# Optimization experiments

Measured on AMD Instinct MI355X. Metric: run time of the kernel, lower is better.

Reference implementation:

```python
import jax, jax.numpy as jnp
import numpy as np

N, C, HI, WI = 8, 3, 512, 512   # src_img NCHW (input_img_size)
HO, WO = 2048, 2048             # output canvas (output_img_size[2:])
EPS = 1e-8


def _transform_one(img, coor_row):
    """Replicates: sigmoid box params -> theta -> F.affine_grid -> F.grid_sample
    (bilinear, zeros padding, align_corners=False). Theta has zero off-diagonals,
    so the grid is separable in x/y and the bilinear sample factorizes.
    img: [C, HI, WI]; coor_row: [4]. Returns (sample [C,HO,WO], mask [HO,WO])."""
    x = jax.nn.sigmoid(coor_row[0]) * WO
    y = jax.nn.sigmoid(coor_row[1]) * HO
    w = jax.nn.sigmoid(coor_row[2]) * WO
    h = jax.nn.sigmoid(coor_row[3]) * HO
    a = WO / (w + EPS)
    tx = 2.0 / WO * (WO / 2.0 - x) * a
    b = HO / (h + EPS)
    ty = 2.0 / HO * (HO / 2.0 - y) * b
    # affine_grid base coords (align_corners=False): center-of-pixel normalized
    xs = (2.0 * jnp.arange(WO, dtype=img.dtype) + 1.0) / WO - 1.0
    ys = (2.0 * jnp.arange(HO, dtype=img.dtype) + 1.0) / HO - 1.0
    gx = a * xs + tx          # [WO]
    gy = b * ys + ty          # [HO]
    # grid_sample unnormalize (align_corners=False)
    ix = ((gx + 1.0) * WI - 1.0) / 2.0
    iy = ((gy + 1.0) * HI - 1.0) / 2.0
    x0f = jnp.floor(ix); y0f = jnp.floor(iy)
    wx1 = ix - x0f; wx0 = 1.0 - wx1
    wy1 = iy - y0f; wy0 = 1.0 - wy1
    x0 = x0f.astype(jnp.int32); x1 = x0 + 1
    y0 = y0f.astype(jnp.int32); y1 = y0 + 1
    vx0 = ((x0 >= 0) & (x0 < WI)).astype(img.dtype)
    vx1 = ((x1 >= 0) & (x1 < WI)).astype(img.dtype)
    vy0 = ((y0 >= 0) & (y0 < HI)).astype(img.dtype)
    vy1 = ((y1 >= 0) & (y1 < HI)).astype(img.dtype)
    x0c = jnp.clip(x0, 0, WI - 1); x1c = jnp.clip(x1, 0, WI - 1)
    y0c = jnp.clip(y0, 0, HI - 1); y1c = jnp.clip(y1, 0, HI - 1)
    wyv0 = wy0 * vy0; wyv1 = wy1 * vy1
    wxv0 = wx0 * vx0; wxv1 = wx1 * vx1
    # separable bilinear gather with zero padding
    rows = img[:, y0c, :] * wyv0[None, :, None] + img[:, y1c, :] * wyv1[None, :, None]  # [C,HO,WI]
    samp = rows[:, :, x0c] * wxv0[None, None, :] + rows[:, :, x1c] * wxv1[None, None, :]  # [C,HO,WO]
    # grid_sample of an all-ones mask == sum of in-bounds bilinear weights (separable)
    mask = (wyv0 + wyv1)[:, None] * (wxv0 + wxv1)[None, :]  # [HO,WO]
    return samp, mask


def _composite(src_img, bg_img, coor):
    def step(bg, inp):
        img, c = inp
        s, m = _transform_one(img, c)
        bg = bg * (1.0 - m)[None, None] + (s * m[None])[None]
        return bg, None
    bg, _ = jax.lax.scan(step, bg_img, (src_img, coor))
    return bg


def setup_inputs() -> dict:
    key = jax.random.key(0)
    k1, k2, k3 = jax.random.split(key, 3)
    src_img = jax.random.normal(k1, (N, C, HI, WI), dtype=jnp.float32)
    bg_img = jax.random.uniform(k2, (1, C, HO, WO), dtype=jnp.float32)
    coor = jax.random.normal(k3, (N, 4), dtype=jnp.float32)  # nn.Parameter
    return {"src_img": src_img, "bg_img": bg_img, "coor": coor}


def reference(src_img, bg_img, coor):
    return _composite(src_img, bg_img, coor)
```

## Files before the change

### kernel.cpp

```cpp
#include <hip/hip_runtime.h>

#define WI 512
#define HI 512
#define WO 2048
#define HO 2048
#define NIMG 8
#define CCH 3
#define EPS 1e-8f
#define PLANE (HI * WI)

#define TPB  256
#define SEG  1024
#define PXT  4
#define CAP  520

struct SState {
    float wy0, wy1, my;
    int   t0a, R, lim;
    int   valid;
    int   fc;
};

__device__ __forceinline__ SState calc_state(const float4 P, const float ys,
                                             const int wo0) {
    SState st; st.valid = 0; st.fc = 0; st.wy0 = st.wy1 = st.my = 0.0f;
    st.t0a = 0; st.R = 0; st.lim = 0;
    const float gy  = P.z * ys + P.w;
    const float iy  = ((gy + 1.0f) * (float)HI - 1.0f) * 0.5f;
    const float y0f = floorf(iy);
    const float fy1 = iy - y0f;
    const float fy0 = 1.0f - fy1;
    const float y1f = y0f + 1.0f;
    const float v0  = (y0f >= 0.0f && y0f < (float)HI) ? 1.0f : 0.0f;
    const float v1  = (y1f >= 0.0f && y1f < (float)HI) ? 1.0f : 0.0f;
    st.wy0 = fy0 * v0;
    st.wy1 = fy1 * v1;
    st.my  = st.wy0 + st.wy1;
    if (!(st.my > 0.0f)) return st;

    const float a  = P.x, tx = P.y;
    const float xsf = (2.0f * (float)wo0 + 1.0f) / (float)WO - 1.0f;
    const float xsl = (2.0f * (float)(wo0 + SEG - 1) + 1.0f) / (float)WO - 1.0f;
    const float ixf = ((a * xsf + tx + 1.0f) * (float)WI - 1.0f) * 0.5f;
    const float ixl = ((a * xsl + tx + 1.0f) * (float)WI - 1.0f) * 0.5f;
    if (ixl <= -1.0f || ixf >= (float)WI) return st;

    const int t0 = (int)fminf(fmaxf(floorf(ixf), 0.0f), (float)(WI - 1));
    const int t1 = (int)fminf(fmaxf(floorf(ixl) + 1.0f, 0.0f), (float)(WI - 1));
    st.t0a = t0 & ~3;
    int R = (t1 - st.t0a + 4) & ~3;
    if (R > WI - st.t0a) R = WI - st.t0a;
    st.R   = R;
    st.lim = t1 - st.t0a;
    st.valid = 1;
    st.fc = (st.my == 1.0f) && (ixf >= 0.0f) && (ixl < (float)(WI - 1));
    return st;
}

__launch_bounds__(TPB)
__global__ void diffcomp_v10(const float* __restrict__ src,
                             const float* __restrict__ bg,
                             const float* __restrict__ coor,
                             float* __restrict__ out) {
    __shared__ float  cs[2][CCH][CAP];
    __shared__ float4 prm[NIMG];

    const int tid = threadIdx.x;
    const int b   = blockIdx.x;
    const int row = b >> 1;
    const int wo0 = (b & 1) << 10;

    if (tid < NIMG) {
        const float cx  = coor[tid * 4 + 0];
        const float cy  = coor[tid * 4 + 1];
        const float cw  = coor[tid * 4 + 2];
        const float chh = coor[tid * 4 + 3];
        const float x = (1.0f / (1.0f + expf(-cx))) * (float)WO;
        const float y = (1.0f / (1.0f + expf(-cy))) * (float)HO;
        const float w = (1.0f / (1.0f + expf(-cw))) * (float)WO;
        const float h = (1.0f / (1.0f + expf(-chh))) * (float)HO;
        const float a  = (float)WO / (w + EPS);
        const float tx = (2.0f / (float)WO) * ((float)WO * 0.5f - x) * a;
        const float bb = (float)HO / (h + EPS);
        const float ty = (2.0f / (float)HO) * ((float)HO * 0.5f - y) * bb;
        prm[tid] = make_float4(a, tx, bb, ty);
    }
    __syncthreads();

    const float ys = (2.0f * (float)row + 1.0f) / (float)HO - 1.0f;

    unsigned cov = 0u, fcb = 0u;
#pragma unroll
    for (int n = 0; n < NIMG; n++) {
        const SState s = calc_state(prm[n], ys, wo0);
        if (s.valid) cov |= (1u << n);
        if (s.fc)    fcb |= (1u << n);
    }
    if (fcb) {
        const int j0 = 31 - __builtin_clz(fcb);
        cov &= ~((1u << j0) - 1u);
    }

    float xsv[PXT];
#pragma unroll
    for (int p = 0; p < PXT; p++) {
        const int wo = wo0 + p * TPB + tid;
        xsv[p] = (2.0f * (float)wo + 1.0f) / (float)WO - 1.0f;
    }

    const int base = row * WO + wo0 + tid;
    float acc[CCH][PXT];
    if (fcb == 0u) {
#pragma unroll
        for (int c = 0; c < CCH; c++)
#pragma unroll
            for (int p = 0; p < PXT; p++)
                acc[c][p] = bg[c * HO * WO + base + p * TPB];
    } else {
#pragma unroll
        for (int c = 0; c < CCH; c++)
#pragma unroll
            for (int p = 0; p < PXT; p++)
                acc[c][p] = 0.0f;
    }

    if (cov) {
        float4 A0[CCH], A1[CCH], B0[CCH], B1[CCH];
        SState stA, stB;

        auto load_img = [&](int n, SState& st, float4* r0, float4* r1) {
            st = calc_state(prm[n], ys, wo0);
            const int xo = tid << 2;
            if (xo < st.R) {
                const float* ib = src + n * (CCH * PLANE) + st.t0a + xo;
                const float gy  = prm[n].z * ys + prm[n].w;
                const float iy  = ((gy + 1.0f) * (float)HI - 1.0f) * 0.5f;
                const float y0f = floorf(iy);
                const int y0o = (int)fminf(fmaxf(y0f, 0.0f), (float)(HI - 1)) * WI;
                const int y1o = (int)fminf(fmaxf(y0f + 1.0f, 0.0f), (float)(HI - 1)) * WI;
#pragma unroll
                for (int c = 0; c < CCH; c++) {
                    r0[c] = *(const float4*)(ib + c * PLANE + y0o);
                    r1[c] = *(const float4*)(ib + c * PLANE + y1o);
                }
            }
        };

        auto commit_img = [&](int slot, const SState& st,
                              const float4* r0, const float4* r1) {
            const int xo = tid << 2;
            if (xo < st.R) {
#pragma unroll
                for (int c = 0; c < CCH; c++) {
                    float4 rc;
                    rc.x = r0[c].x * st.wy0 + r1[c].x * st.wy1;
                    rc.y = r0[c].y * st.wy0 + r1[c].y * st.wy1;
                    rc.z = r0[c].z * st.wy0 + r1[c].z * st.wy1;
                    rc.w = r0[c].w * st.wy0 + r1[c].w * st.wy1;
                    *(float4*)&cs[slot][c][xo] = rc;
                }
            }
        };

        auto blend_img = [&](int slot, int n, const SState& st) {
            const float a  = prm[n].x;
            const float tx = prm[n].y;
#pragma unroll
            for (int p = 0; p < PXT; p++) {
                const float gx  = a * xsv[p] + tx;
                const float ix  = ((gx + 1.0f) * (float)WI - 1.0f) * 0.5f;
                const float x0f = floorf(ix);
                const float fx1 = ix - x0f;
                const float fx0 = 1.0f - fx1;
                const float x1f = x0f + 1.0f;
                const float v0  = (x0f >= 0.0f && x0f < (float)WI) ? 1.0f : 0.0f;
                const float v1  = (x1f >= 0.0f && x1f < (float)WI) ? 1.0f : 0.0f;
                const float wx0 = fx0 * v0;
                const float wx1 = fx1 * v1;
                int x0r = (int)fminf(fmaxf(x0f, 0.0f), (float)(WI - 1)) - st.t0a;
                int x1r = (int)fminf(fmaxf(x1f, 0.0f), (float)(WI - 1)) - st.t0a;
                x0r = min(max(x0r, 0), st.lim);
                x1r = min(max(x1r, 0), st.lim);
                const float m  = st.my * (wx0 + wx1);
                const float om = 1.0f - m;
#pragma unroll
                for (int c = 0; c < CCH; c++) {
                    const float q0 = cs[slot][c][x0r];
                    const float q1 = cs[slot][c][x1r];
                    const float sc = q0 * wx0 + q1 * wx1;
                    acc[c][p] = acc[c][p] * om + sc * m;
                }
            }
        };

        int cur = (int)__builtin_ctz(cov);
        unsigned rest = cov & (cov - 1u);

        load_img(cur, stA, A0, A1);
        int s = 0;
        while (true) {
            const int nxt = rest ? (int)__builtin_ctz(rest) : -1;
            if (nxt >= 0) load_img(nxt, stB, B0, B1);
            commit_img(s, stA, A0, A1);
            __syncthreads();
            blend_img(s, cur, stA);
            if (nxt < 0) break;
            cur = nxt;
            rest &= rest - 1u;
            stA = stB;
#pragma unroll
            for (int c = 0; c < CCH; c++) { A0[c] = B0[c]; A1[c] = B1[c]; }
            s ^= 1;
        }
    }

#pragma unroll
    for (int c = 0; c < CCH; c++)
#pragma unroll
        for (int p = 0; p < PXT; p++)
            out[c * HO * WO + base + p * TPB] = acc[c][p];
}

extern "C" void kernel_launch(void* const* d_in, const int* in_sizes, int n_in,
                              void* d_out, int out_size, void* d_ws, size_t ws_size,
                              hipStream_t stream) {
    const float* src  = (const float*)d_in[0];
    const float* bg   = (const float*)d_in[1];
    const float* coor = (const float*)d_in[2];
    float* out = (float*)d_out;
    (void)d_ws; (void)ws_size;

    hipLaunchKernelGGL(diffcomp_v10, dim3(HO * (WO / SEG)), dim3(TPB), 0, stream,
                       src, bg, coor, out);
}
```

Measured before the change: 134.9 us.

## Precompute per-image row state in LDS, vectorize pixel IO, interleave channels

```diff
diff --git a/kernel.cpp b/kernel.cpp
--- a/kernel.cpp
+++ b/kernel.cpp
@@ -14,108 +14,95 @@
 #define PXT  4
 #define CAP  520
 
-struct SState {
-    float wy0, wy1, my;
-    int   t0a, R, lim;
-    int   valid;
-    int   fc;
-};
-
-__device__ __forceinline__ SState calc_state(const float4 P, const float ys,
-                                             const int wo0) {
-    SState st; st.valid = 0; st.fc = 0; st.wy0 = st.wy1 = st.my = 0.0f;
-    st.t0a = 0; st.R = 0; st.lim = 0;
-    const float gy  = P.z * ys + P.w;
-    const float iy  = ((gy + 1.0f) * (float)HI - 1.0f) * 0.5f;
-    const float y0f = floorf(iy);
-    const float fy1 = iy - y0f;
-    const float fy0 = 1.0f - fy1;
-    const float y1f = y0f + 1.0f;
-    const float v0  = (y0f >= 0.0f && y0f < (float)HI) ? 1.0f : 0.0f;
-    const float v1  = (y1f >= 0.0f && y1f < (float)HI) ? 1.0f : 0.0f;
-    st.wy0 = fy0 * v0;
-    st.wy1 = fy1 * v1;
-    st.my  = st.wy0 + st.wy1;
-    if (!(st.my > 0.0f)) return st;
-
-    const float a  = P.x, tx = P.y;
-    const float xsf = (2.0f * (float)wo0 + 1.0f) / (float)WO - 1.0f;
-    const float xsl = (2.0f * (float)(wo0 + SEG - 1) + 1.0f) / (float)WO - 1.0f;
-    const float ixf = ((a * xsf + tx + 1.0f) * (float)WI - 1.0f) * 0.5f;
-    const float ixl = ((a * xsl + tx + 1.0f) * (float)WI - 1.0f) * 0.5f;
-    if (ixl <= -1.0f || ixf >= (float)WI) return st;
-
-    const int t0 = (int)fminf(fmaxf(floorf(ixf), 0.0f), (float)(WI - 1));
-    const int t1 = (int)fminf(fmaxf(floorf(ixl) + 1.0f, 0.0f), (float)(WI - 1));
-    st.t0a = t0 & ~3;
-    int R = (t1 - st.t0a + 4) & ~3;
-    if (R > WI - st.t0a) R = WI - st.t0a;
-    st.R   = R;
-    st.lim = t1 - st.t0a;
-    st.valid = 1;
-    st.fc = (st.my == 1.0f) && (ixf >= 0.0f) && (ixl < (float)(WI - 1));
-    return st;
-}
-
 __launch_bounds__(TPB)
-__global__ void diffcomp_v10(const float* __restrict__ src,
+__global__ void diffcomp_v11(const float* __restrict__ src,
                              const float* __restrict__ bg,
                              const float* __restrict__ coor,
                              float* __restrict__ out) {
-    __shared__ float  cs[2][CCH][CAP];
-    __shared__ float4 prm[NIMG];
+    __shared__ __align__(16) float cs[2][CAP * CCH];
+    __shared__ float4 st1[NIMG];
+    __shared__ float4 st2[NIMG];
+    __shared__ float4 st3[NIMG];
 
     const int tid = threadIdx.x;
-    const int b   = blockIdx.x;
+    const int b0  = blockIdx.x;
+    const int b   = ((b0 & 7) << 9) | (b0 >> 3);
     const int row = b >> 1;
     const int wo0 = (b & 1) << 10;
+    const float ys = (2.0f * (float)row + 1.0f) / (float)HO - 1.0f;
+    const float HW1 = 0.5f * (float)(WI - 1);
 
     if (tid < NIMG) {
         const float cx  = coor[tid * 4 + 0];
         const float cy  = coor[tid * 4 + 1];
         const float cw  = coor[tid * 4 + 2];
         const float chh = coor[tid * 4 + 3];
-        const float x = (1.0f / (1.0f + expf(-cx))) * (float)WO;
-        const float y = (1.0f / (1.0f + expf(-cy))) * (float)HO;
-        const float w = (1.0f / (1.0f + expf(-cw))) * (float)WO;
-        const float h = (1.0f / (1.0f + expf(-chh))) * (float)HO;
+        const float xx = (1.0f / (1.0f + expf(-cx))) * (float)WO;
+        const float yy = (1.0f / (1.0f + expf(-cy))) * (float)HO;
+        const float w  = (1.0f / (1.0f + expf(-cw))) * (float)WO;
+        const float h  = (1.0f / (1.0f + expf(-chh))) * (float)HO;
         const float a  = (float)WO / (w + EPS);
-        const float tx = (2.0f / (float)WO) * ((float)WO * 0.5f - x) * a;
         const float bb = (float)HO / (h + EPS);
-        const float ty = (2.0f / (float)HO) * ((float)HO * 0.5f - y) * bb;
-        prm[tid] = make_float4(a, tx, bb, ty);
+        const float ty = (2.0f / (float)HO) * ((float)HO * 0.5f - yy) * bb;
+
+        const float gy  = bb * ys + ty;
+        const float iy  = ((gy + 1.0f) * (float)HI - 1.0f) * 0.5f;
+        const float y0f = floorf(iy);
+        const float fy1 = iy - y0f;
+        const float fy0 = 1.0f - fy1;
+        const float y1f = y0f + 1.0f;
+        const float v0  = (y0f >= 0.0f && y0f < (float)HI) ? 1.0f : 0.0f;
+        const float v1  = (y1f >= 0.0f && y1f < (float)HI) ? 1.0f : 0.0f;
+        const float wy0 = fy0 * v0;
+        const float wy1 = fy1 * v1;
+        const float my  = wy0 + wy1;
+        const float y0of = fminf(fmaxf(y0f, 0.0f), (float)(HI - 1)) * (float)WI;
+        const float y1of = fminf(fmaxf(y1f, 0.0f), (float)(HI - 1)) * (float)WI;
+
+        const float A2 = a * ((float)WI / (float)WO);
+        const float D  = 0.5f - xx;
+
+        float myv = 0.0f, t0af = 0.0f, limf = 0.0f, Rf = 0.0f, fcf = 0.0f;
+        if (my > 0.0f) {
+            const float ixf = fmaf(A2, (float)wo0 + D, HW1);
+            const float ixl = fmaf(A2, (float)(wo0 + SEG - 1) + D, HW1);
+            if (!(ixl <= -1.0f || ixf >= (float)WI)) {
+                const int t0 = (int)fminf(fmaxf(floorf(ixf), 0.0f), (float)(WI - 1));
+                const int t1 = (int)fminf(fmaxf(floorf(ixl) + 1.0f, 0.0f), (float)(WI - 1));
+                const int t0a = t0 & ~3;
+                int R = (t1 - t0a + 4) & ~3;
+                if (R > WI - t0a) R = WI - t0a;
+                myv = my; t0af = (float)t0a; limf = (float)(t1 - t0a); Rf = (float)R;
+                fcf = (my == 1.0f && ixf >= 0.0f && ixl < (float)(WI - 1)) ? 1.0f : 0.0f;
+            }
+        }
+        st1[tid] = make_float4(myv, t0af, limf, Rf);
+        st2[tid] = make_float4(wy0, wy1, y0of, y1of);
+        st3[tid] = make_float4(A2, D, fcf, 0.0f);
     }
     __syncthreads();
 
-    const float ys = (2.0f * (float)row + 1.0f) / (float)HO - 1.0f;
-
     unsigned cov = 0u, fcb = 0u;
 #pragma unroll
     for (int n = 0; n < NIMG; n++) {
-        const SState s = calc_state(prm[n], ys, wo0);
-        if (s.valid) cov |= (1u << n);
-        if (s.fc)    fcb |= (1u << n);
+        if (st1[n].w > 0.0f) cov |= (1u << n);
+        if (st3[n].z > 0.0f) fcb |= (1u << n);
     }
     if (fcb) {
         const int j0 = 31 - __builtin_clz(fcb);
         cov &= ~((1u << j0) - 1u);
     }
 
-    float xsv[PXT];
-#pragma unroll
-    for (int p = 0; p < PXT; p++) {
-        const int wo = wo0 + p * TPB + tid;
-        xsv[p] = (2.0f * (float)wo + 1.0f) / (float)WO - 1.0f;
-    }
-
-    const int base = row * WO + wo0 + tid;
+    const int px0   = wo0 + (tid << 2);
+    const int gbase = row * WO + px0;
+
     float acc[CCH][PXT];
     if (fcb == 0u) {
 #pragma unroll
-        for (int c = 0; c < CCH; c++)
-#pragma unroll
-            for (int p = 0; p < PXT; p++)
-                acc[c][p] = bg[c * HO * WO + base + p * TPB];
+        for (int c = 0; c < CCH; c++) {
+            const float4 bv = *(const float4*)&bg[c * (HO * WO) + gbase];
+            acc[c][0] = bv.x; acc[c][1] = bv.y; acc[c][2] = bv.z; acc[c][3] = bv.w;
+        }
     } else {
 #pragma unroll
         for (int c = 0; c < CCH; c++)
@@ -126,18 +113,16 @@
 
     if (cov) {
         float4 A0[CCH], A1[CCH], B0[CCH], B1[CCH];
-        SState stA, stB;
-
-        auto load_img = [&](int n, SState& st, float4* r0, float4* r1) {
-            st = calc_state(prm[n], ys, wo0);
+        float4 s1A, s2A, s3A, s1B, s2B, s3B;
+
+        auto load_img = [&](int n, float4& s1, float4& s2, float4& s3,
+                            float4* r0, float4* r1) {
+            s1 = st1[n]; s2 = st2[n]; s3 = st3[n];
             const int xo = tid << 2;
-            if (xo < st.R) {
-                const float* ib = src + n * (CCH * PLANE) + st.t0a + xo;
-                const float gy  = prm[n].z * ys + prm[n].w;
-                const float iy  = ((gy + 1.0f) * (float)HI - 1.0f) * 0.5f;
-                const float y0f = floorf(iy);
-                const int y0o = (int)fminf(fmaxf(y0f, 0.0f), (float)(HI - 1)) * WI;
-                const int y1o = (int)fminf(fmaxf(y0f + 1.0f, 0.0f), (float)(HI - 1)) * WI;
+            if (xo < (int)s1.w) {
+                const float* ib = src + n * (CCH * PLANE) + (int)s1.y + xo;
+                const int y0o = (int)s2.z;
+                const int y1o = (int)s2.w;
 #pragma unroll
                 for (int c = 0; c < CCH; c++) {
                     r0[c] = *(const float4*)(ib + c * PLANE + y0o);
@@ -146,49 +131,93 @@
             }
         };
 
-        auto commit_img = [&](int slot, const SState& st,
+        auto commit_img = [&](int slot, const float4 s1, const float4 s2,
                               const float4* r0, const float4* r1) {
             const int xo = tid << 2;
-            if (xo < st.R) {
-#pragma unroll
-                for (int c = 0; c < CCH; c++) {
-                    float4 rc;
-                    rc.x = r0[c].x * st.wy0 + r1[c].x * st.wy1;
-                    rc.y = r0[c].y * st.wy0 + r1[c].y * st.wy1;
-                    rc.z = r0[c].z * st.wy0 + r1[c].z * st.wy1;
-                    rc.w = r0[c].w * st.wy0 + r1[c].w * st.wy1;
-                    *(float4*)&cs[slot][c][xo] = rc;
+            if (xo < (int)s1.w) {
+                const float wy0 = s2.x, wy1 = s2.y;
+                float wv[12];
+#pragma unroll
+                for (int t = 0; t < 4; t++)
+#pragma unroll
+                    for (int c = 0; c < CCH; c++)
+                        wv[t * CCH + c] = ((const float*)&r0[c])[t] * wy0
+                                        + ((const float*)&r1[c])[t] * wy1;
+                float* dst = &cs[slot][xo * CCH];
+                ((float4*)dst)[0] = make_float4(wv[0], wv[1], wv[2],  wv[3]);
+                ((float4*)dst)[1] = make_float4(wv[4], wv[5], wv[6],  wv[7]);
+                ((float4*)dst)[2] = make_float4(wv[8], wv[9], wv[10], wv[11]);
+            }
+        };
+
+        auto blend_img = [&](int slot, const float4 s1, const float4 s3) {
+            const float my = s1.x, t0af = s1.y;
+            const float A2 = s3.x, D = s3.y;
+            const float* ls = &cs[slot][0];
+            const int pw0 = wo0 + ((tid >> 6) << 8);
+            const float ixF = fmaf(A2, (float)pw0 + D, HW1);
+            const float ixL = fmaf(A2, (float)(pw0 + 255) + D, HW1);
+            if (ixL <= -1.0f || ixF >= (float)WI) return;
+            if (ixF >= 0.0f && ixL < (float)(WI - 1)) {
+                const float omy = 1.0f - my;
+                if (omy == 0.0f) {
+#pragma unroll
+                    for (int p = 0; p < PXT; p++) {
+                        const float ix  = fmaf(A2, (float)(px0 + p) + D, HW1);
+                        const float x0f = floorf(ix);
+                        const float fx1 = ix - x0f;
+                        const int   k   = (int)(x0f - t0af);
+                        const float* tp = ls + k * CCH;
+#pragma unroll
+                        for (int c = 0; c < CCH; c++) {
+                            const float q0 = tp[c];
+                            const float q1 = tp[c + CCH];
+                            acc[c][p] = q0 + fx1 * (q1 - q0);
+                        }
+                    }
+                } else {
+#pragma unroll
+                    for (int p = 0; p < PXT; p++) {
+                        const float ix  = fmaf(A2, (float)(px0 + p) + D, HW1);
+                        const float x0f = floorf(ix);
+                        const float fx1 = ix - x0f;
+                        const int   k   = (int)(x0f - t0af);
+                        const float* tp = ls + k * CCH;
+#pragma unroll
+                        for (int c = 0; c < CCH; c++) {
+                            const float q0 = tp[c];
+                            const float q1 = tp[c + CCH];
+                            const float sc = q0 + fx1 * (q1 - q0);
+                            acc[c][p] = acc[c][p] * omy + my * sc;
+                        }
+                    }
                 }
-            }
-        };
-
-        auto blend_img = [&](int slot, int n, const SState& st) {
-            const float a  = prm[n].x;
-            const float tx = prm[n].y;
-#pragma unroll
-            for (int p = 0; p < PXT; p++) {
-                const float gx  = a * xsv[p] + tx;
-                const float ix  = ((gx + 1.0f) * (float)WI - 1.0f) * 0.5f;
-                const float x0f = floorf(ix);
-                const float fx1 = ix - x0f;
-                const float fx0 = 1.0f - fx1;
-                const float x1f = x0f + 1.0f;
-                const float v0  = (x0f >= 0.0f && x0f < (float)WI) ? 1.0f : 0.0f;
-                const float v1  = (x1f >= 0.0f && x1f < (float)WI) ? 1.0f : 0.0f;
-                const float wx0 = fx0 * v0;
-                const float wx1 = fx1 * v1;
-                int x0r = (int)fminf(fmaxf(x0f, 0.0f), (float)(WI - 1)) - st.t0a;
-                int x1r = (int)fminf(fmaxf(x1f, 0.0f), (float)(WI - 1)) - st.t0a;
-                x0r = min(max(x0r, 0), st.lim);
-                x1r = min(max(x1r, 0), st.lim);
-                const float m  = st.my * (wx0 + wx1);
-                const float om = 1.0f - m;
-#pragma unroll
-                for (int c = 0; c < CCH; c++) {
-                    const float q0 = cs[slot][c][x0r];
-                    const float q1 = cs[slot][c][x1r];
-                    const float sc = q0 * wx0 + q1 * wx1;
-                    acc[c][p] = acc[c][p] * om + sc * m;
+            } else {
+                const int lim = (int)s1.z;
+                const int t0a = (int)t0af;
+#pragma unroll
+                for (int p = 0; p < PXT; p++) {
+                    const float ix  = fmaf(A2, (float)(px0 + p) + D, HW1);
+                    const float x0f = floorf(ix);
+                    const float fx1 = ix - x0f;
+                    const float fx0 = 1.0f - fx1;
+                    const float x1f = x0f + 1.0f;
+                    const float v0  = (x0f >= 0.0f && x0f < (float)WI) ? 1.0f : 0.0f;
+                    const float v1  = (x1f >= 0.0f && x1f < (float)WI) ? 1.0f : 0.0f;
+                    const float wx0 = fx0 * v0;
+                    const float wx1 = fx1 * v1;
+                    int x0r = (int)fminf(fmaxf(x0f, 0.0f), (float)(WI - 1)) - t0a;
+                    int x1r = (int)fminf(fmaxf(x1f, 0.0f), (float)(WI - 1)) - t0a;
+                    x0r = min(max(x0r, 0), lim);
+                    x1r = min(max(x1r, 0), lim);
+                    const float m  = my * (wx0 + wx1);
+                    const float om = 1.0f - m;
+#pragma unroll
+                    for (int c = 0; c < CCH; c++) {
+                        const float q0 = ls[x0r * CCH + c];
+                        const float q1 = ls[x1r * CCH + c];
+                        acc[c][p] = acc[c][p] * om + (q0 * wx0 + q1 * wx1) * m;
+                    }
                 }
             }
         };
@@ -196,18 +225,18 @@
         int cur = (int)__builtin_ctz(cov);
         unsigned rest = cov & (cov - 1u);
 
-        load_img(cur, stA, A0, A1);
+        load_img(cur, s1A, s2A, s3A, A0, A1);
         int s = 0;
         while (true) {
             const int nxt = rest ? (int)__builtin_ctz(rest) : -1;
-            if (nxt >= 0) load_img(nxt, stB, B0, B1);
-            commit_img(s, stA, A0, A1);
+            if (nxt >= 0) load_img(nxt, s1B, s2B, s3B, B0, B1);
+            commit_img(s, s1A, s2A, A0, A1);
             __syncthreads();
-            blend_img(s, cur, stA);
+            blend_img(s, s1A, s3A);
             if (nxt < 0) break;
             cur = nxt;
             rest &= rest - 1u;
-            stA = stB;
+            s1A = s1B; s2A = s2B; s3A = s3B;
 #pragma unroll
             for (int c = 0; c < CCH; c++) { A0[c] = B0[c]; A1[c] = B1[c]; }
             s ^= 1;
@@ -216,9 +245,8 @@
 
 #pragma unroll
     for (int c = 0; c < CCH; c++)
-#pragma unroll
-        for (int p = 0; p < PXT; p++)
-            out[c * HO * WO + base + p * TPB] = acc[c][p];
+        *(float4*)&out[c * (HO * WO) + gbase] =
+            make_float4(acc[c][0], acc[c][1], acc[c][2], acc[c][3]);
 }
 
 extern "C" void kernel_launch(void* const* d_in, const int* in_sizes, int n_in,
@@ -230,6 +258,6 @@
     float* out = (float*)d_out;
     (void)d_ws; (void)ws_size;
 
-    hipLaunchKernelGGL(diffcomp_v10, dim3(HO * (WO / SEG)), dim3(TPB), 0, stream,
+    hipLaunchKernelGGL(diffcomp_v11, dim3(HO * (WO / SEG)), dim3(TPB), 0, stream,
                        src, bg, coor, out);
 }
```

Measured after the change: 134.1 us. No clear change (-0.5%).
